# Kernel optimization log

Hardware: AMD Instinct MI355X
Metric: run time of the kernel (lower is better)

The kernel has to match this reference:

```python
import jax, jax.numpy as jnp
import numpy as np
import math

B, C, H, T, S = 2, 1024, 16, 2048, 2048
DH = C // H  # 64


def setup_inputs() -> dict:
    key = jax.random.key(0)
    ks = jax.random.split(key, 10)
    target = jax.random.normal(ks[0], (B, C, T), dtype=jnp.float32)
    source = jax.random.normal(ks[1], (B, C, S), dtype=jnp.float32)
    target_mask = (jax.random.uniform(ks[2], (B, 1, T)) < 0.9).astype(jnp.float32)
    source_mask = (jax.random.uniform(ks[3], (B, 1, S)) < 0.9).astype(jnp.float32)
    scale = 1.0 / math.sqrt(C)
    Wq = jax.random.normal(ks[4], (C, C), dtype=jnp.float32) * scale
    bq = jnp.zeros((C,), dtype=jnp.float32)
    Wk = jax.random.normal(ks[5], (C, C), dtype=jnp.float32) * scale
    bk = jnp.zeros((C,), dtype=jnp.float32)
    Wv = jax.random.normal(ks[6], (C, C), dtype=jnp.float32) * scale
    bv = jnp.zeros((C,), dtype=jnp.float32)
    return {"target": target, "source": source, "target_mask": target_mask,
            "source_mask": source_mask, "Wq": Wq, "bq": bq, "Wk": Wk, "bk": bk,
            "Wv": Wv, "bv": bv}


def _proj(W, b, x):
    # 1x1 Conv1d == pointwise channel mixing: [B,C,L] -> [B,C,L]
    return jnp.einsum('oc,bcl->bol', W, x) + b[None, :, None]


def reference(target, source, target_mask, source_mask, Wq, bq, Wk, bk, Wv, bv):
    q = _proj(Wq, bq, target).reshape(B, H, DH, T)
    k = _proj(Wk, bk, source).reshape(B, H, DH, S)
    v = _proj(Wv, bv, source).reshape(B, H, DH, S)
    # dot: [B,H,T,S], scaled by sqrt(d_head) (key.size(2) in torch)
    dot = jnp.einsum('bhdt,bhds->bhts', q, k) / math.sqrt(DH)
    # available mask [B,1,T,S], broadcast over heads
    avail = jnp.einsum('bjt,bjs->bjts', target_mask, source_mask)
    dot = avail * dot - (1.0 - avail) * 1.0e6
    # NOTE: original torch code overwrites the masked amap with a plain
    # softmax of the (masked) dot; we reproduce that exactly.
    amap = jax.nn.softmax(dot, axis=-1)
    out = jnp.einsum('bhts,bhds->bhdt', amap, v)  # [B,H,DH,T]
    return out.reshape(B, C, T)
```

## Files before the change

### kernel.cpp

```cpp
#include <hip/hip_runtime.h>

#define BB 2
#define CC 1024
#define HH 16
#define TT 2048
#define SS 2048
#define LL 2048
#define C2MASK 1442695.0f

typedef unsigned short u16;
typedef unsigned int u32;
typedef __attribute__((ext_vector_type(8))) short short8;
typedef __attribute__((ext_vector_type(4))) float f32x4;
typedef __attribute__((ext_vector_type(4))) unsigned short us4;
typedef __attribute__((ext_vector_type(2))) unsigned int u32x2;
typedef __attribute__((ext_vector_type(4))) unsigned int u32x4;

__device__ __forceinline__ u16 f2bf(float f) {
    union { float f; unsigned int i; } x; x.f = f;
    unsigned int r = x.i + 0x7FFFu + ((x.i >> 16) & 1u);
    return (u16)(r >> 16);
}
__device__ __forceinline__ float exp2_hw(float x) {
    float r;
    asm("v_exp_f32 %0, %1" : "=v"(r) : "v"(x));
    return r;
}
__device__ __forceinline__ float max3f(float a, float b, float c) {
    float r;
    asm("v_max3_f32 %0, %1, %2, %3" : "=v"(r) : "v"(a), "v"(b), "v"(c));
    return r;
}
__device__ __forceinline__ u32 cvtpk_bf16(float lo, float hi) {
    u32 r;
    asm("v_cvt_pk_bf16_f32 %0, %1, %2" : "=v"(r) : "v"(lo), "v"(hi));
    return r;
}
__device__ __forceinline__ void gload_lds16(const u16* g, u16* l) {
    __builtin_amdgcn_global_load_lds(
        (const __attribute__((address_space(1))) unsigned int*)g,
        (__attribute__((address_space(3))) unsigned int*)l, 16, 0, 0);
}

__global__ __launch_bounds__(256) void prep(
    const float* __restrict__ target, const float* __restrict__ source,
    const float* __restrict__ smaskp,
    const float* __restrict__ Wq, const float* __restrict__ Wk, const float* __restrict__ Wv,
    u16* __restrict__ Wb, u16* __restrict__ Tt, u16* __restrict__ St,
    float* __restrict__ sbias, float* __restrict__ zrow)
{
    __shared__ float xs[64][65];
    const int tid = threadIdx.x;
    const int bid = blockIdx.x;

    if (bid < 2048) {
        const int img  = bid >> 9;
        const int tile = bid & 511;
        const int ct = tile >> 5, lt = tile & 31;
        const int c0 = ct * 64, l0 = lt * 64;
        const float* src = ((img < 2) ? target : source) + (size_t)(img & 1) * CC * LL;
        u16* dst = ((img < 2) ? Tt : St) + (size_t)(img & 1) * LL * CC;

        const int i = tid >> 2, seg = (tid & 3) * 16;
        const float* g = src + (size_t)(c0 + i) * LL + l0 + seg;
        f32x4 a0 = *(const f32x4*)g;
        f32x4 a1 = *(const f32x4*)(g + 4);
        f32x4 a2 = *(const f32x4*)(g + 8);
        f32x4 a3 = *(const f32x4*)(g + 12);
#pragma unroll
        for (int j = 0; j < 4; j++) {
            xs[i][seg + j]      = a0[j];
            xs[i][seg + 4 + j]  = a1[j];
            xs[i][seg + 8 + j]  = a2[j];
            xs[i][seg + 12 + j] = a3[j];
        }
        __syncthreads();

        const int l = tid >> 2, cseg = (tid & 3) * 16;
        float f[16];
#pragma unroll
        for (int j = 0; j < 16; j++) f[j] = xs[cseg + j][l];
        u32x4 o0, o1;
#pragma unroll
        for (int k = 0; k < 4; k++) {
            o0[k] = cvtpk_bf16(f[2 * k], f[2 * k + 1]);
            o1[k] = cvtpk_bf16(f[8 + 2 * k], f[9 + 2 * k]);
        }
        u16* d = dst + (size_t)(l0 + l) * CC + c0 + cseg;
        *(u32x4*)d = o0;
        *(u32x4*)(d + 8) = o1;
    } else {
        const int wblk = bid - 2048;
        const size_t idx = (size_t)wblk * 2048 + tid * 8;
        const int m = (int)(idx >> 20);
        const size_t rem = idx & 1048575;
        const float* srcp = ((m == 0) ? Wq : (m == 1) ? Wk : Wv) + rem;
        f32x4 a = *(const f32x4*)srcp;
        f32x4 c = *(const f32x4*)(srcp + 4);
        u32x4 o;
        o[0] = cvtpk_bf16(a[0], a[1]); o[1] = cvtpk_bf16(a[2], a[3]);
        o[2] = cvtpk_bf16(c[0], c[1]); o[3] = cvtpk_bf16(c[2], c[3]);
        *(u32x4*)(Wb + ((size_t)m << 20) + rem) = o;

        if (wblk < 2) {
            const int b = wblk;
            const float* sm = smaskp + (size_t)b * SS;
            float* sb = sbias + (size_t)b * SS;
            for (int s = tid; s < SS; s += 256) {
                sb[s] = (sm[s] > 0.5f) ? 0.0f : -C2MASK;
                if (b == 0) zrow[s] = 0.0f;
            }
        }
    }
}

__global__ __launch_bounds__(512, 2) void qkv_gemm(
    const u16* __restrict__ Wb, const u16* __restrict__ Tt, const u16* __restrict__ St,
    const float* __restrict__ bq, const float* __restrict__ bk, const float* __restrict__ bv,
    const float* __restrict__ tmaskp,
    u16* __restrict__ Qb, u16* __restrict__ Kb, u16* __restrict__ Vb)
{
    __shared__ __align__(16) u16 As[2][16384];
    __shared__ __align__(16) u16 Bs[2][16384];

    const int orig = blockIdx.x;
    const int wg   = (orig & 7) * 24 + (orig >> 3);
    const int mT   = wg >> 4;
    const int nT   = wg & 15;
    const int m0 = mT * 256;
    const int n0 = nT * 256;
    const int p  = m0 >> 10;

    const u16* A  = Wb + (size_t)m0 * CC;
    const u16* Bx = ((p == 0) ? Tt : St) + (size_t)n0 * CC;
    const float* bias = (p == 0) ? bq : (p == 1) ? bk : bv;

    const int tid  = threadIdx.x;
    const int lane = tid & 63;
    const int wid  = tid >> 6;
    const int ln   = lane & 15;
    const int q    = lane >> 4;
    const int wm   = (wid >> 2) * 128;
    const int wn   = (wid & 3) * 64;

    const u16* ag[4]; const u16* bg[4];
#pragma unroll
    for (int e = 0; e < 4; e++) {
        const int s = tid + e * 512;
        const int row = s >> 3;
        const int c = (s & 7) ^ (row & 7);
        ag[e] = A  + (size_t)row * CC + c * 8;
        bg[e] = Bx + (size_t)row * CC + c * 8;
    }
    const int lw = wid * 512;

#define STG_A(buf, k0, e)  gload_lds16(ag[e] + (k0), &As[buf][(e) * 4096 + lw])
#define STG_B(buf, k0, e)  gload_lds16(bg[e] + (k0), &Bs[buf][(e) * 4096 + lw])

    f32x4 acc[8][4];
#pragma unroll
    for (int i = 0; i < 8; i++)
#pragma unroll
        for (int j = 0; j < 4; j++) acc[i][j] = (f32x4){0.f, 0.f, 0.f, 0.f};

    const int sx0 = ((q ^ (ln & 7)) << 3);
    const int sx1 = (((q + 4) ^ (ln & 7)) << 3);

    short8 aQ[4][2];
    short8 bQ[2][2][2];

#define PH_READ_A(cb, base_mt) do {                                        \
    _Pragma("unroll") for (int mt = 0; mt < 4; mt++) {                     \
        const u16* ar = &As[cb][(wm + ((base_mt) + mt) * 16 + ln) * 64];   \
        aQ[mt][0] = *(const short8*)(ar + sx0);                            \
        aQ[mt][1] = *(const short8*)(ar + sx1); } } while (0)
#define PH_READ_B(cb, ntg) do {                                            \
    _Pragma("unroll") for (int nt = 0; nt < 2; nt++) {                     \
        const u16* br = &Bs[cb][(wn + ((ntg) * 2 + nt) * 16 + ln) * 64];   \
        bQ[ntg][nt][0] = *(const short8*)(br + sx0);                       \
        bQ[ntg][nt][1] = *(const short8*)(br + sx1); } } while (0)
#define PH_MFMA(mbase, ntg) do {                                           \
    __builtin_amdgcn_s_setprio(1);                                         \
    _Pragma("unroll") for (int mt = 0; mt < 4; mt++)                       \
    _Pragma("unroll") for (int nt = 0; nt < 2; nt++) {                     \
        acc[(mbase) + mt][(ntg) * 2 + nt] = __builtin_amdgcn_mfma_f32_16x16x32_bf16( \
            aQ[mt][0], bQ[ntg][nt][0], acc[(mbase) + mt][(ntg) * 2 + nt], 0, 0, 0);  \
        acc[(mbase) + mt][(ntg) * 2 + nt] = __builtin_amdgcn_mfma_f32_16x16x32_bf16( \
            aQ[mt][1], bQ[ntg][nt][1], acc[(mbase) + mt][(ntg) * 2 + nt], 0, 0, 0); } \
    __builtin_amdgcn_s_setprio(0); } while (0)
#define LGKM0 do { asm volatile("s_waitcnt lgkmcnt(0)" ::: "memory");      \
                   __builtin_amdgcn_sched_barrier(0); } while (0)
#define VMDRAIN do { asm volatile("s_waitcnt vmcnt(0)" ::: "memory");      \
                     __builtin_amdgcn_sched_barrier(0); } while (0)

    STG_A(0, 0, 0); STG_A(0, 0, 1); STG_A(0, 0, 2); STG_A(0, 0, 3);
    STG_B(0, 0, 0); STG_B(0, 0, 1); STG_B(0, 0, 2); STG_B(0, 0, 3);
    __syncthreads();

#pragma unroll 1
    for (int T = 0; T < 16; ++T) {
        const int c  = T & 1;
        const int kn = (T + 1) * 64;
        const bool stg = (T < 15);

        PH_READ_A(c, 0); PH_READ_B(c, 0);
        if (stg) { STG_A(c ^ 1, kn, 0); STG_A(c ^ 1, kn, 1);
                   STG_A(c ^ 1, kn, 2); STG_A(c ^ 1, kn, 3); }
        __builtin_amdgcn_s_barrier(); LGKM0; PH_MFMA(0, 0);
        __builtin_amdgcn_s_barrier();

        PH_READ_B(c, 1);
        if (stg) { STG_B(c ^ 1, kn, 0); STG_B(c ^ 1, kn, 1);
                   STG_B(c ^ 1, kn, 2); STG_B(c ^ 1, kn, 3); }
        __builtin_amdgcn_s_barrier(); LGKM0; PH_MFMA(0, 1);
        __builtin_amdgcn_s_barrier();

        PH_READ_A(c, 4);
        __builtin_amdgcn_s_barrier(); LGKM0; PH_MFMA(4, 0);
        __builtin_amdgcn_s_barrier();

        PH_MFMA(4, 1);
        VMDRAIN;
        __builtin_amdgcn_s_barrier();
    }
#undef VMDRAIN
#undef LGKM0
#undef PH_MFMA
#undef PH_READ_B
#undef PH_READ_A
#undef STG_B
#undef STG_A

    const float oscale = 0.18033688011112042f;
#pragma unroll
    for (int mt = 0; mt < 8; mt++) {
        const int o_base = (m0 & 1023) + wm + mt * 16 + q * 4;
        float bsf[4];
#pragma unroll
        for (int r = 0; r < 4; r++) bsf[r] = bias[o_base + r];
#pragma unroll
        for (int nt = 0; nt < 4; nt++) {
            const int l  = n0 + wn + nt * 16 + ln;
            const int b  = l >> 11;
            const int tk = l & 2047;
            if (p == 2) {
#pragma unroll
                for (int r = 0; r < 4; r++)
                    Vb[((size_t)b * CC + o_base + r) * SS + tk] = f2bf(acc[mt][nt][r] + bsf[r]);
            } else {
                const int h = o_base >> 6;
                const int d = o_base & 63;
                u16* dst = (p == 0) ? Qb : Kb;
                float sc2 = 1.0f;
                if (p == 0) sc2 = oscale * tmaskp[(size_t)b * TT + tk];
                us4 pk;
#pragma unroll
                for (int r = 0; r < 4; r++) pk[r] = (u16)f2bf((acc[mt][nt][r] + bsf[r]) * sc2);
                *(us4*)(dst + ((size_t)(b * HH + h) * TT + tk) * 64 + d) = pk;
            }
        }
    }
}

__global__ __launch_bounds__(512, 4) void attn_k(
    const u16* __restrict__ Qb, const u16* __restrict__ Kb, const u16* __restrict__ Vb,
    const float* __restrict__ tmask, const float* __restrict__ sbias,
    const float* __restrict__ zrow, float* __restrict__ out)
{
    __shared__ __align__(16) u16 Ks[2][128 * 64];
    __shared__ __align__(16) u16 Vs[2][2][64 * 64];
    __shared__ __align__(16) u16 Ps[8][16 * 64];

    const int tid  = threadIdx.x;
    const int wid  = tid >> 6;
    const int lane = tid & 63;
    const int ln   = lane & 15;
    const int q    = lane >> 4;

    const int idx   = blockIdx.x;
    const int xcd   = idx & 7;
    const int rest  = idx >> 3;
    const int ttile = rest & 15;
    const int bh    = (rest >> 4) * 8 + xcd;
    const int b     = bh >> 4;
    const int h     = bh & 15;
    const int t0    = ttile * 128 + wid * 16;

    const u16* Qp = Qb + (size_t)bh * TT * 64;
    const u16* Kp = Kb + (size_t)bh * SS * 64;
    const u16* Vp = Vb + ((size_t)b * CC + h * 64) * SS;

    const float tm = tmask[(size_t)b * TT + t0 + ln];
    const float* bp = (tm > 0.5f) ? (sbias + (size_t)b * SS) : zrow;

    const int rk = tid >> 3;
    const int ck = (tid & 7) ^ (rk & 7);
    const u16* kg  = Kp + (size_t)rk * 64 + ck * 8;
    const u16* kg2 = kg + 64 * 64;
    const u16* vg = Vp + (size_t)rk * SS + ck * 8;
    const int lws = wid * 512;

#define STAGE(buf, sn) do {                                        \
        gload_lds16(kg  + (size_t)(sn) * 64, &Ks[buf][lws]);       \
        gload_lds16(kg2 + (size_t)(sn) * 64, &Ks[buf][4096 + lws]);\
        gload_lds16(vg  + (sn),      &Vs[buf][0][lws]);            \
        gload_lds16(vg  + (sn) + 64, &Vs[buf][1][lws]);            \
    } while (0)

    short8 qB0 = *(const short8*)(Qp + (size_t)(t0 + ln) * 64 + q * 8);
    short8 qB1 = *(const short8*)(Qp + (size_t)(t0 + ln) * 64 + 32 + q * 8);

    float mR = -3.0e38f, lR = 0.f;
    f32x4 oA[4];
#pragma unroll
    for (int dt = 0; dt < 4; dt++) oA[dt] = (f32x4){0.f, 0.f, 0.f, 0.f};

    const int sx0 = ((q ^ (ln & 7)) << 3);
    const int sx1 = (((q + 4) ^ (ln & 7)) << 3);

    u16* pw = Ps[wid];

    STAGE(0, 0);

    f32x4 bR[8];
#pragma unroll
    for (int nt = 0; nt < 8; nt++)
        bR[nt] = *(const f32x4*)(bp + nt * 16 + q * 4);

    int cur = 0;
#pragma unroll 2
    for (int w = 0; w < 16; ++w) {
        const int s0 = w * 128;
        __syncthreads();
        if (w + 1 < 16) STAGE(cur ^ 1, s0 + 128);

        const u16* KsB = Ks[cur];

        f32x4 sc[8];
        __builtin_amdgcn_s_setprio(1);
#pragma unroll
        for (int nt = 0; nt < 8; nt++) {
            const u16* kr = KsB + (nt * 16 + ln) * 64;
            short8 k0 = *(const short8*)(kr + sx0);
            short8 k1 = *(const short8*)(kr + sx1);
            sc[nt] = __builtin_amdgcn_mfma_f32_16x16x32_bf16(k0, qB0, bR[nt], 0, 0, 0);
            sc[nt] = __builtin_amdgcn_mfma_f32_16x16x32_bf16(k1, qB1, sc[nt], 0, 0, 0);
        }
        __builtin_amdgcn_s_setprio(0);

        {
            const int snx = (w + 1 < 16) ? s0 + 128 : s0;
#pragma unroll
            for (int nt = 0; nt < 8; nt++)
                bR[nt] = *(const f32x4*)(bp + snx + nt * 16 + q * 4);
        }

        float m4[8];
#pragma unroll
        for (int nt = 0; nt < 8; nt++)
            m4[nt] = fmaxf(max3f(sc[nt][0], sc[nt][1], sc[nt][2]), sc[nt][3]);
        float t1 = max3f(m4[0], m4[1], m4[2]);
        float t2 = max3f(m4[3], m4[4], m4[5]);
        float t3 = fmaxf(m4[6], m4[7]);
        float m_ = max3f(t1, t2, t3);
        m_ = fmaxf(m_, __shfl_xor(m_, 16, 64));
        m_ = fmaxf(m_, __shfl_xor(m_, 32, 64));

        if (!__all(m_ - mR <= 8.0f)) {
            const float mN = fmaxf(mR, m_);
            const float al = exp2_hw(mR - mN);
            lR *= al;
#pragma unroll
            for (int dt = 0; dt < 4; dt++) oA[dt] *= al;
            mR = mN;
        }

        float ssum = 0.f;
#pragma unroll
        for (int nt = 0; nt < 8; nt++) {
#pragma unroll
            for (int r = 0; r < 4; r++) sc[nt][r] = exp2_hw(sc[nt][r] - mR);
            ssum += (sc[nt][0] + sc[nt][1]) + (sc[nt][2] + sc[nt][3]);
        }
        lR += ssum;

#pragma unroll
        for (int nt = 0; nt < 4; nt++) {
            u32x2 wv;
            wv[0] = cvtpk_bf16(sc[nt][0], sc[nt][1]);
            wv[1] = cvtpk_bf16(sc[nt][2], sc[nt][3]);
            const int chunk = (nt << 1) | (q >> 1);
            *(u32x2*)(pw + ln * 64 + ((chunk ^ (ln & 7)) << 3) + ((q & 1) << 2)) = wv;
        }
        {
            const u16* VsH = Vs[cur][0];
            short8 pB0 = *(const short8*)(pw + ln * 64 + sx0);
            short8 pB1 = *(const short8*)(pw + ln * 64 + sx1);
            __builtin_amdgcn_s_setprio(1);
#pragma unroll
            for (int dt = 0; dt < 4; dt++) {
                const u16* vr = VsH + (dt * 16 + ln) * 64;
                short8 v0 = *(const short8*)(vr + sx0);
                short8 v1 = *(const short8*)(vr + sx1);
                oA[dt] = __builtin_amdgcn_mfma_f32_16x16x32_bf16(v0, pB0, oA[dt], 0, 0, 0);
                oA[dt] = __builtin_amdgcn_mfma_f32_16x16x32_bf16(v1, pB1, oA[dt], 0, 0, 0);
            }
            __builtin_amdgcn_s_setprio(0);
        }
#pragma unroll
        for (int nt = 0; nt < 4; nt++) {
            u32x2 wv;
            wv[0] = cvtpk_bf16(sc[4 + nt][0], sc[4 + nt][1]);
            wv[1] = cvtpk_bf16(sc[4 + nt][2], sc[4 + nt][3]);
            const int chunk = (nt << 1) | (q >> 1);
            *(u32x2*)(pw + ln * 64 + ((chunk ^ (ln & 7)) << 3) + ((q & 1) << 2)) = wv;
        }
        {
            const u16* VsH = Vs[cur][1];
            short8 pB0 = *(const short8*)(pw + ln * 64 + sx0);
            short8 pB1 = *(const short8*)(pw + ln * 64 + sx1);
            __builtin_amdgcn_s_setprio(1);
#pragma unroll
            for (int dt = 0; dt < 4; dt++) {
                const u16* vr = VsH + (dt * 16 + ln) * 64;
                short8 v0 = *(const short8*)(vr + sx0);
                short8 v1 = *(const short8*)(vr + sx1);
                oA[dt] = __builtin_amdgcn_mfma_f32_16x16x32_bf16(v0, pB0, oA[dt], 0, 0, 0);
                oA[dt] = __builtin_amdgcn_mfma_f32_16x16x32_bf16(v1, pB1, oA[dt], 0, 0, 0);
            }
            __builtin_amdgcn_s_setprio(0);
        }
        cur ^= 1;
    }
#undef STAGE

    lR += __shfl_xor(lR, 16, 64);
    lR += __shfl_xor(lR, 32, 64);
    const float inv = 1.0f / lR;
#pragma unroll
    for (int dt = 0; dt < 4; dt++)
#pragma unroll
        for (int r = 0; r < 4; r++)
            out[((size_t)b * CC + h * 64 + dt * 16 + q * 4 + r) * TT + t0 + ln] =
                oA[dt][r] * inv;
}

extern "C" void kernel_launch(void* const* d_in, const int* in_sizes, int n_in,
                              void* d_out, int out_size, void* d_ws, size_t ws_size,
                              hipStream_t stream)
{
    const float* target = (const float*)d_in[0];
    const float* source = (const float*)d_in[1];
    const float* tmask  = (const float*)d_in[2];
    const float* smask  = (const float*)d_in[3];
    const float* Wq = (const float*)d_in[4];
    const float* bq = (const float*)d_in[5];
    const float* Wk = (const float*)d_in[6];
    const float* bk = (const float*)d_in[7];
    const float* Wv = (const float*)d_in[8];
    const float* bv = (const float*)d_in[9];

    u16* ws = (u16*)d_ws;
    const size_t N1 = (size_t)BB * CC * TT;
    u16* Qb = ws;
    u16* Kb = ws + N1;
    u16* Vb = ws + 2 * N1;
    float* sbias = (float*)(ws + 3 * N1);
    float* zrow  = sbias + 2 * SS;
    u16* Wb = (u16*)(zrow + SS);
    u16* Tt = Wb + 3u * 1048576u;
    u16* St = Tt + (size_t)BB * LL * CC;

    prep<<<dim3(3584, 1, 1), dim3(256, 1, 1), 0, stream>>>(
        target, source, smask, Wq, Wk, Wv, Wb, Tt, St, sbias, zrow);
    qkv_gemm<<<dim3(192, 1, 1), dim3(512, 1, 1), 0, stream>>>(
        Wb, Tt, St, bq, bk, bv, tmask, Qb, Kb, Vb);
    attn_k<<<dim3(BB*HH*(TT/128), 1, 1), dim3(512, 1, 1), 0, stream>>>(
        Qb, Kb, Vb, tmask, sbias, zrow, (float*)d_out);
}
```

Measured before the change: 203.3 us.

## Give each attention wave two 16-row query tiles to reuse K/V fragments

```diff
diff --git a/kernel.cpp b/kernel.cpp
--- a/kernel.cpp
+++ b/kernel.cpp
@@ -262,14 +262,14 @@
     }
 }
 
-__global__ __launch_bounds__(512, 4) void attn_k(
+__global__ __launch_bounds__(256, 2) void attn_k(
     const u16* __restrict__ Qb, const u16* __restrict__ Kb, const u16* __restrict__ Vb,
     const float* __restrict__ tmask, const float* __restrict__ sbias,
     const float* __restrict__ zrow, float* __restrict__ out)
 {
     __shared__ __align__(16) u16 Ks[2][128 * 64];
     __shared__ __align__(16) u16 Vs[2][2][64 * 64];
-    __shared__ __align__(16) u16 Ps[8][16 * 64];
+    __shared__ __align__(16) u16 Ps[4][16 * 64];
 
     const int tid  = threadIdx.x;
     const int wid  = tid >> 6;
@@ -284,36 +284,56 @@
     const int bh    = (rest >> 4) * 8 + xcd;
     const int b     = bh >> 4;
     const int h     = bh & 15;
-    const int t0    = ttile * 128 + wid * 16;
+    const int t0    = ttile * 128 + wid * 32;
 
     const u16* Qp = Qb + (size_t)bh * TT * 64;
     const u16* Kp = Kb + (size_t)bh * SS * 64;
     const u16* Vp = Vb + ((size_t)b * CC + h * 64) * SS;
 
-    const float tm = tmask[(size_t)b * TT + t0 + ln];
-    const float* bp = (tm > 0.5f) ? (sbias + (size_t)b * SS) : zrow;
-
-    const int rk = tid >> 3;
-    const int ck = (tid & 7) ^ (rk & 7);
-    const u16* kg  = Kp + (size_t)rk * 64 + ck * 8;
-    const u16* kg2 = kg + 64 * 64;
-    const u16* vg = Vp + (size_t)rk * SS + ck * 8;
+    const float tmA = tmask[(size_t)b * TT + t0 + ln];
+    const float tmB = tmask[(size_t)b * TT + t0 + 16 + ln];
+    const float* bpA = (tmA > 0.5f) ? (sbias + (size_t)b * SS) : zrow;
+    const float* bpB = (tmB > 0.5f) ? (sbias + (size_t)b * SS) : zrow;
+
+    const u16* kg[4];
+#pragma unroll
+    for (int e = 0; e < 4; e++) {
+        const int c = tid + e * 256;
+        const int row = c >> 3;
+        const int col = (c & 7) ^ (row & 7);
+        kg[e] = Kp + (size_t)row * 64 + col * 8;
+    }
+    const u16* vg[2];
+#pragma unroll
+    for (int e = 0; e < 2; e++) {
+        const int c = tid + e * 256;
+        const int dr = c >> 3;
+        const int col = (c & 7) ^ (dr & 7);
+        vg[e] = Vp + (size_t)dr * SS + col * 8;
+    }
     const int lws = wid * 512;
 
-#define STAGE(buf, sn) do {                                        \
-        gload_lds16(kg  + (size_t)(sn) * 64, &Ks[buf][lws]);       \
-        gload_lds16(kg2 + (size_t)(sn) * 64, &Ks[buf][4096 + lws]);\
-        gload_lds16(vg  + (sn),      &Vs[buf][0][lws]);            \
-        gload_lds16(vg  + (sn) + 64, &Vs[buf][1][lws]);            \
+#define STAGE(buf, sn) do {                                                   \
+        gload_lds16(kg[0] + (size_t)(sn) * 64, &Ks[buf][lws]);                \
+        gload_lds16(kg[1] + (size_t)(sn) * 64, &Ks[buf][2048 + lws]);         \
+        gload_lds16(kg[2] + (size_t)(sn) * 64, &Ks[buf][4096 + lws]);         \
+        gload_lds16(kg[3] + (size_t)(sn) * 64, &Ks[buf][6144 + lws]);         \
+        gload_lds16(vg[0] + (sn),      &Vs[buf][0][lws]);                     \
+        gload_lds16(vg[1] + (sn),      &Vs[buf][0][2048 + lws]);              \
+        gload_lds16(vg[0] + (sn) + 64, &Vs[buf][1][lws]);                     \
+        gload_lds16(vg[1] + (sn) + 64, &Vs[buf][1][2048 + lws]);              \
     } while (0)
 
-    short8 qB0 = *(const short8*)(Qp + (size_t)(t0 + ln) * 64 + q * 8);
-    short8 qB1 = *(const short8*)(Qp + (size_t)(t0 + ln) * 64 + 32 + q * 8);
-
-    float mR = -3.0e38f, lR = 0.f;
-    f32x4 oA[4];
-#pragma unroll
-    for (int dt = 0; dt < 4; dt++) oA[dt] = (f32x4){0.f, 0.f, 0.f, 0.f};
+    short8 qA0 = *(const short8*)(Qp + (size_t)(t0 + ln) * 64 + q * 8);
+    short8 qA1 = *(const short8*)(Qp + (size_t)(t0 + ln) * 64 + 32 + q * 8);
+    short8 qC0 = *(const short8*)(Qp + (size_t)(t0 + 16 + ln) * 64 + q * 8);
+    short8 qC1 = *(const short8*)(Qp + (size_t)(t0 + 16 + ln) * 64 + 32 + q * 8);
+
+    float mRA = -3.0e38f, lRA = 0.f;
+    float mRB = -3.0e38f, lRB = 0.f;
+    f32x4 oA[4], oB[4];
+#pragma unroll
+    for (int dt = 0; dt < 4; dt++) { oA[dt] = (f32x4){0.f,0.f,0.f,0.f}; oB[dt] = (f32x4){0.f,0.f,0.f,0.f}; }
 
     const int sx0 = ((q ^ (ln & 7)) << 3);
     const int sx1 = (((q + 4) ^ (ln & 7)) << 3);
@@ -322,13 +342,8 @@
 
     STAGE(0, 0);
 
-    f32x4 bR[8];
-#pragma unroll
-    for (int nt = 0; nt < 8; nt++)
-        bR[nt] = *(const f32x4*)(bp + nt * 16 + q * 4);
-
     int cur = 0;
-#pragma unroll 2
+#pragma unroll 1
     for (int w = 0; w < 16; ++w) {
         const int s0 = w * 128;
         __syncthreads();
@@ -336,113 +351,133 @@
 
         const u16* KsB = Ks[cur];
 
-        f32x4 sc[8];
+        f32x4 sA[8], sB[8];
         __builtin_amdgcn_s_setprio(1);
 #pragma unroll
         for (int nt = 0; nt < 8; nt++) {
             const u16* kr = KsB + (nt * 16 + ln) * 64;
             short8 k0 = *(const short8*)(kr + sx0);
             short8 k1 = *(const short8*)(kr + sx1);
-            sc[nt] = __builtin_amdgcn_mfma_f32_16x16x32_bf16(k0, qB0, bR[nt], 0, 0, 0);
-            sc[nt] = __builtin_amdgcn_mfma_f32_16x16x32_bf16(k1, qB1, sc[nt], 0, 0, 0);
+            f32x4 bA = *(const f32x4*)(bpA + s0 + nt * 16 + q * 4);
+            f32x4 bB = *(const f32x4*)(bpB + s0 + nt * 16 + q * 4);
+            sA[nt] = __builtin_amdgcn_mfma_f32_16x16x32_bf16(k0, qA0, bA, 0, 0, 0);
+            sA[nt] = __builtin_amdgcn_mfma_f32_16x16x32_bf16(k1, qA1, sA[nt], 0, 0, 0);
+            sB[nt] = __builtin_amdgcn_mfma_f32_16x16x32_bf16(k0, qC0, bB, 0, 0, 0);
+            sB[nt] = __builtin_amdgcn_mfma_f32_16x16x32_bf16(k1, qC1, sB[nt], 0, 0, 0);
         }
         __builtin_amdgcn_s_setprio(0);
 
+        float mA_, mB_;
         {
-            const int snx = (w + 1 < 16) ? s0 + 128 : s0;
+            float m4[8];
 #pragma unroll
             for (int nt = 0; nt < 8; nt++)
-                bR[nt] = *(const f32x4*)(bp + snx + nt * 16 + q * 4);
-        }
-
-        float m4[8];
-#pragma unroll
-        for (int nt = 0; nt < 8; nt++)
-            m4[nt] = fmaxf(max3f(sc[nt][0], sc[nt][1], sc[nt][2]), sc[nt][3]);
-        float t1 = max3f(m4[0], m4[1], m4[2]);
-        float t2 = max3f(m4[3], m4[4], m4[5]);
-        float t3 = fmaxf(m4[6], m4[7]);
-        float m_ = max3f(t1, t2, t3);
-        m_ = fmaxf(m_, __shfl_xor(m_, 16, 64));
-        m_ = fmaxf(m_, __shfl_xor(m_, 32, 64));
-
-        if (!__all(m_ - mR <= 8.0f)) {
-            const float mN = fmaxf(mR, m_);
-            const float al = exp2_hw(mR - mN);
-            lR *= al;
-#pragma unroll
-            for (int dt = 0; dt < 4; dt++) oA[dt] *= al;
-            mR = mN;
-        }
-
-        float ssum = 0.f;
+                m4[nt] = fmaxf(max3f(sA[nt][0], sA[nt][1], sA[nt][2]), sA[nt][3]);
+            mA_ = max3f(max3f(m4[0], m4[1], m4[2]), max3f(m4[3], m4[4], m4[5]), fmaxf(m4[6], m4[7]));
+            mA_ = fmaxf(mA_, __shfl_xor(mA_, 16, 64));
+            mA_ = fmaxf(mA_, __shfl_xor(mA_, 32, 64));
+        }
+        {
+            float m4[8];
+#pragma unroll
+            for (int nt = 0; nt < 8; nt++)
+                m4[nt] = fmaxf(max3f(sB[nt][0], sB[nt][1], sB[nt][2]), sB[nt][3]);
+            mB_ = max3f(max3f(m4[0], m4[1], m4[2]), max3f(m4[3], m4[4], m4[5]), fmaxf(m4[6], m4[7]));
+            mB_ = fmaxf(mB_, __shfl_xor(mB_, 16, 64));
+            mB_ = fmaxf(mB_, __shfl_xor(mB_, 32, 64));
+        }
+
+        if (!__all((mA_ - mRA <= 8.0f) && (mB_ - mRB <= 8.0f))) {
+            const float mNA = fmaxf(mRA, mA_);
+            const float mNB = fmaxf(mRB, mB_);
+            const float alA = exp2_hw(mRA - mNA);
+            const float alB = exp2_hw(mRB - mNB);
+            lRA *= alA; lRB *= alB;
+#pragma unroll
+            for (int dt = 0; dt < 4; dt++) { oA[dt] *= alA; oB[dt] *= alB; }
+            mRA = mNA; mRB = mNB;
+        }
+
+        float ssA = 0.f, ssB = 0.f;
 #pragma unroll
         for (int nt = 0; nt < 8; nt++) {
 #pragma unroll
-            for (int r = 0; r < 4; r++) sc[nt][r] = exp2_hw(sc[nt][r] - mR);
-            ssum += (sc[nt][0] + sc[nt][1]) + (sc[nt][2] + sc[nt][3]);
-        }
-        lR += ssum;
-
-#pragma unroll
-        for (int nt = 0; nt < 4; nt++) {
-            u32x2 wv;
-            wv[0] = cvtpk_bf16(sc[nt][0], sc[nt][1]);
-            wv[1] = cvtpk_bf16(sc[nt][2], sc[nt][3]);
-            const int chunk = (nt << 1) | (q >> 1);
-            *(u32x2*)(pw + ln * 64 + ((chunk ^ (ln & 7)) << 3) + ((q & 1) << 2)) = wv;
-        }
-        {
-            const u16* VsH = Vs[cur][0];
-            short8 pB0 = *(const short8*)(pw + ln * 64 + sx0);
-            short8 pB1 = *(const short8*)(pw + ln * 64 + sx1);
-            __builtin_amdgcn_s_setprio(1);
+            for (int r = 0; r < 4; r++) {
+                sA[nt][r] = exp2_hw(sA[nt][r] - mRA);
+                sB[nt][r] = exp2_hw(sB[nt][r] - mRB);
+            }
+            ssA += (sA[nt][0] + sA[nt][1]) + (sA[nt][2] + sA[nt][3]);
+            ssB += (sB[nt][0] + sB[nt][1]) + (sB[nt][2] + sB[nt][3]);
+        }
+        lRA += ssA; lRB += ssB;
+
+#pragma unroll
+        for (int sh = 0; sh < 2; sh++) {
+            const u16* VsH = Vs[cur][sh];
+            short8 v[4][2];
 #pragma unroll
             for (int dt = 0; dt < 4; dt++) {
                 const u16* vr = VsH + (dt * 16 + ln) * 64;
-                short8 v0 = *(const short8*)(vr + sx0);
-                short8 v1 = *(const short8*)(vr + sx1);
-                oA[dt] = __builtin_amdgcn_mfma_f32_16x16x32_bf16(v0, pB0, oA[dt], 0, 0, 0);
-                oA[dt] = __builtin_amdgcn_mfma_f32_16x16x32_bf16(v1, pB1, oA[dt], 0, 0, 0);
-            }
-            __builtin_amdgcn_s_setprio(0);
-        }
-#pragma unroll
-        for (int nt = 0; nt < 4; nt++) {
-            u32x2 wv;
-            wv[0] = cvtpk_bf16(sc[4 + nt][0], sc[4 + nt][1]);
-            wv[1] = cvtpk_bf16(sc[4 + nt][2], sc[4 + nt][3]);
-            const int chunk = (nt << 1) | (q >> 1);
-            *(u32x2*)(pw + ln * 64 + ((chunk ^ (ln & 7)) << 3) + ((q & 1) << 2)) = wv;
-        }
-        {
-            const u16* VsH = Vs[cur][1];
-            short8 pB0 = *(const short8*)(pw + ln * 64 + sx0);
-            short8 pB1 = *(const short8*)(pw + ln * 64 + sx1);
-            __builtin_amdgcn_s_setprio(1);
-#pragma unroll
-            for (int dt = 0; dt < 4; dt++) {
-                const u16* vr = VsH + (dt * 16 + ln) * 64;
-                short8 v0 = *(const short8*)(vr + sx0);
-                short8 v1 = *(const short8*)(vr + sx1);
-                oA[dt] = __builtin_amdgcn_mfma_f32_16x16x32_bf16(v0, pB0, oA[dt], 0, 0, 0);
-                oA[dt] = __builtin_amdgcn_mfma_f32_16x16x32_bf16(v1, pB1, oA[dt], 0, 0, 0);
-            }
-            __builtin_amdgcn_s_setprio(0);
+                v[dt][0] = *(const short8*)(vr + sx0);
+                v[dt][1] = *(const short8*)(vr + sx1);
+            }
+#pragma unroll
+            for (int nt = 0; nt < 4; nt++) {
+                u32x2 wv;
+                wv[0] = cvtpk_bf16(sA[sh * 4 + nt][0], sA[sh * 4 + nt][1]);
+                wv[1] = cvtpk_bf16(sA[sh * 4 + nt][2], sA[sh * 4 + nt][3]);
+                const int chunk = (nt << 1) | (q >> 1);
+                *(u32x2*)(pw + ln * 64 + ((chunk ^ (ln & 7)) << 3) + ((q & 1) << 2)) = wv;
+            }
+            {
+                short8 pB0 = *(const short8*)(pw + ln * 64 + sx0);
+                short8 pB1 = *(const short8*)(pw + ln * 64 + sx1);
+                __builtin_amdgcn_s_setprio(1);
+#pragma unroll
+                for (int dt = 0; dt < 4; dt++) {
+                    oA[dt] = __builtin_amdgcn_mfma_f32_16x16x32_bf16(v[dt][0], pB0, oA[dt], 0, 0, 0);
+                    oA[dt] = __builtin_amdgcn_mfma_f32_16x16x32_bf16(v[dt][1], pB1, oA[dt], 0, 0, 0);
+                }
+                __builtin_amdgcn_s_setprio(0);
+            }
+#pragma unroll
+            for (int nt = 0; nt < 4; nt++) {
+                u32x2 wv;
+                wv[0] = cvtpk_bf16(sB[sh * 4 + nt][0], sB[sh * 4 + nt][1]);
+                wv[1] = cvtpk_bf16(sB[sh * 4 + nt][2], sB[sh * 4 + nt][3]);
+                const int chunk = (nt << 1) | (q >> 1);
+                *(u32x2*)(pw + ln * 64 + ((chunk ^ (ln & 7)) << 3) + ((q & 1) << 2)) = wv;
+            }
+            {
+                short8 pB0 = *(const short8*)(pw + ln * 64 + sx0);
+                short8 pB1 = *(const short8*)(pw + ln * 64 + sx1);
+                __builtin_amdgcn_s_setprio(1);
+#pragma unroll
+                for (int dt = 0; dt < 4; dt++) {
+                    oB[dt] = __builtin_amdgcn_mfma_f32_16x16x32_bf16(v[dt][0], pB0, oB[dt], 0, 0, 0);
+                    oB[dt] = __builtin_amdgcn_mfma_f32_16x16x32_bf16(v[dt][1], pB1, oB[dt], 0, 0, 0);
+                }
+                __builtin_amdgcn_s_setprio(0);
+            }
         }
         cur ^= 1;
     }
 #undef STAGE
 
-    lR += __shfl_xor(lR, 16, 64);
-    lR += __shfl_xor(lR, 32, 64);
-    const float inv = 1.0f / lR;
+    lRA += __shfl_xor(lRA, 16, 64);
+    lRA += __shfl_xor(lRA, 32, 64);
+    lRB += __shfl_xor(lRB, 16, 64);
+    lRB += __shfl_xor(lRB, 32, 64);
+    const float invA = 1.0f / lRA;
+    const float invB = 1.0f / lRB;
 #pragma unroll
     for (int dt = 0; dt < 4; dt++)
 #pragma unroll
-        for (int r = 0; r < 4; r++)
-            out[((size_t)b * CC + h * 64 + dt * 16 + q * 4 + r) * TT + t0 + ln] =
-                oA[dt][r] * inv;
+        for (int r = 0; r < 4; r++) {
+            const size_t rowo = ((size_t)b * CC + h * 64 + dt * 16 + q * 4 + r) * TT;
+            out[rowo + t0 + ln]      = oA[dt][r] * invA;
+            out[rowo + t0 + 16 + ln] = oB[dt][r] * invB;
+        }
 }
 
 extern "C" void kernel_launch(void* const* d_in, const int* in_sizes, int n_in,
@@ -475,6 +510,6 @@
         target, source, smask, Wq, Wk, Wv, Wb, Tt, St, sbias, zrow);
     qkv_gemm<<<dim3(192, 1, 1), dim3(512, 1, 1), 0, stream>>>(
         Wb, Tt, St, bq, bk, bv, tmask, Qb, Kb, Vb);
-    attn_k<<<dim3(BB*HH*(TT/128), 1, 1), dim3(512, 1, 1), 0, stream>>>(
+    attn_k<<<dim3(BB*HH*(TT/128), 1, 1), dim3(256, 1, 1), 0, stream>>>(
         Qb, Kb, Vb, tmask, sbias, zrow, (float*)d_out);
 }
```

New measurement: 207.6 us. +2.1%, slower.
